# Kernel optimization log

Hardware: AMD Instinct MI355X
Metric: run time of the kernel (lower is better)

Reference implementation:

```python
import jax, jax.numpy as jnp
import numpy as np

DIM = 768
N_HEADS = 12
HEAD_DIM = DIM // N_HEADS
MLP_MULT = 4
EPS = 1e-5


def setup_inputs() -> dict:
    key = jax.random.key(0)
    ks = jax.random.split(key, 8)
    B, T = 2, 4096
    s = lambda fan_in: 1.0 / np.sqrt(fan_in)
    return {
        "x": jax.random.normal(ks[0], (B, T, DIM), dtype=jnp.float32),
        "ln1_w": jnp.ones((DIM,), jnp.float32),
        "ln1_b": jnp.zeros((DIM,), jnp.float32),
        # weights stored as (in, out): y = x @ W + b (equivalent to torch Linear)
        "w_qkv": jax.random.normal(ks[1], (DIM, 3 * DIM), jnp.float32) * s(DIM),
        "w_proj": jax.random.normal(ks[2], (DIM, DIM), jnp.float32) * s(DIM),
        "b_proj": jnp.zeros((DIM,), jnp.float32),
        "ln2_w": jnp.ones((DIM,), jnp.float32),
        "ln2_b": jnp.zeros((DIM,), jnp.float32),
        "w1": jax.random.normal(ks[3], (DIM, MLP_MULT * DIM), jnp.float32) * s(DIM),
        "b1": jnp.zeros((MLP_MULT * DIM,), jnp.float32),
        "w2": jax.random.normal(ks[4], (MLP_MULT * DIM, DIM), jnp.float32) * s(MLP_MULT * DIM),
        "b2": jnp.zeros((DIM,), jnp.float32),
    }


def _layernorm(x, w, b):
    mean = jnp.mean(x, axis=-1, keepdims=True)
    var = jnp.var(x, axis=-1, keepdims=True)
    return w * (x - mean) * jax.lax.rsqrt(var + EPS) + b


def reference(x, ln1_w, ln1_b, w_qkv, w_proj, b_proj, ln2_w, ln2_b, w1, b1, w2, b2):
    B, T, C = x.shape
    scale = HEAD_DIM ** -0.5

    # --- attention sub-block (pre-LN) ---
    h = _layernorm(x, ln1_w, ln1_b)
    qkv = h @ w_qkv                               # [B, T, 3C]
    q, k, v = jnp.split(qkv, 3, axis=-1)
    to_heads = lambda t: t.reshape(B, T, N_HEADS, HEAD_DIM).transpose(0, 2, 1, 3)
    q, k, v = to_heads(q), to_heads(k), to_heads(v)  # [B, H, T, D]

    att = jnp.einsum("bhqd,bhkd->bhqk", q, k) * scale  # full T x T scores
    causal = jnp.tril(jnp.ones((T, T), dtype=bool))
    att = jnp.where(causal, att, -jnp.inf)
    att = jax.nn.softmax(att, axis=-1)
    y = jnp.einsum("bhqk,bhkd->bhqd", att, v)          # [B, H, T, D]
    y = y.transpose(0, 2, 1, 3).reshape(B, T, C)
    y = y @ w_proj + b_proj
    x = x + y

    # --- MLP sub-block (pre-LN) ---
    h = _layernorm(x, ln2_w, ln2_b)
    h = jax.nn.gelu(h @ w1 + b1, approximate=False)
    h = h @ w2 + b2
    return x + h
```

## Files before the change

kernel.cpp:

```cpp
#include <hip/hip_runtime.h>

typedef unsigned short u16;
typedef __attribute__((ext_vector_type(4))) unsigned short u16x4;
typedef __attribute__((ext_vector_type(8))) short short8;
typedef __attribute__((ext_vector_type(4))) float f32x4;
typedef __attribute__((ext_vector_type(16))) float f32x16;

#define MFMA32(a, b, c) __builtin_amdgcn_mfma_f32_32x32x16_bf16(a, b, c, 0, 0, 0)

__device__ __forceinline__ u16 f2bf(float f) {
  union { float f; unsigned u; } x; x.f = f;
  unsigned r = x.u + 0x7fffu + ((x.u >> 16) & 1u);
  return (u16)(r >> 16);
}

__device__ __forceinline__ unsigned cvt_pk_bf16(float lo, float hi) {
  unsigned r;
  asm("v_cvt_pk_bf16_f32 %0, %1, %2" : "=v"(r) : "v"(lo), "v"(hi));
  return r;
}

__device__ __forceinline__ void load_lds16(const void* g, void* l) {
  __builtin_amdgcn_global_load_lds(
      (const __attribute__((address_space(1))) void*)g,
      (__attribute__((address_space(3))) void*)l,
      16, 0, 0);
}

__global__ __launch_bounds__(256) void transpose_k(const float* __restrict__ in,
                                                   u16* __restrict__ out,
                                                   int R, int C) {
  __shared__ float tile[32][33];
  const int tx = threadIdx.x & 31, ty = threadIdx.x >> 5;
  const int c0 = blockIdx.x * 32, r0 = blockIdx.y * 32;
#pragma unroll
  for (int i = 0; i < 4; ++i)
    tile[ty + i * 8][tx] = in[(size_t)(r0 + ty + i * 8) * C + c0 + tx];
  __syncthreads();
#pragma unroll
  for (int i = 0; i < 4; ++i)
    out[(size_t)(c0 + ty + i * 8) * R + r0 + tx] = f2bf(tile[tx][ty + i * 8]);
}

__global__ __launch_bounds__(256) void ln_k(const float* __restrict__ X,
                                            const float* __restrict__ w,
                                            const float* __restrict__ b,
                                            u16* __restrict__ O) {
  const int row = blockIdx.x;
  const float* xr = X + (size_t)row * 768;
  const int tid = threadIdx.x;
  float v0 = xr[tid], v1 = xr[tid + 256], v2 = xr[tid + 512];
  float s = v0 + v1 + v2;
  float s2 = v0 * v0 + v1 * v1 + v2 * v2;
#pragma unroll
  for (int m = 32; m; m >>= 1) { s += __shfl_xor(s, m); s2 += __shfl_xor(s2, m); }
  __shared__ float ps[4], ps2[4];
  if ((tid & 63) == 0) { ps[tid >> 6] = s; ps2[tid >> 6] = s2; }
  __syncthreads();
  s = ps[0] + ps[1] + ps[2] + ps[3];
  s2 = ps2[0] + ps2[1] + ps2[2] + ps2[3];
  const float mean = s * (1.f / 768.f);
  const float var = s2 * (1.f / 768.f) - mean * mean;
  const float rstd = rsqrtf(var + 1e-5f);
  u16* orow = O + (size_t)row * 768;
  orow[tid]       = f2bf((v0 - mean) * rstd * w[tid]       + b[tid]);
  orow[tid + 256] = f2bf((v1 - mean) * rstd * w[tid + 256] + b[tid + 256]);
  orow[tid + 512] = f2bf((v2 - mean) * rstd * w[tid + 512] + b[tid + 512]);
}

#define BM 128
#define BN 128
#define BKK 64

template <int EPI>
__global__ __launch_bounds__(256, 2) void gemm_k(
    const u16* __restrict__ A, const u16* __restrict__ Bt, int K, int N,
    const float* __restrict__ bias, const float* __restrict__ res,
    float* __restrict__ outF, u16* __restrict__ outB,
    u16* __restrict__ qout, u16* __restrict__ kout, u16* __restrict__ vout) {
  __shared__ __align__(16) u16 sA[BM * BKK];
  __shared__ __align__(16) u16 sB[BN * BKK];
  const int nTn = N / BN;
  const int nwg = gridDim.x;
  const int bid = ((int)blockIdx.x & 7) * (nwg >> 3) + ((int)blockIdx.x >> 3);
  const int tm = bid / nTn, tn = bid % nTn;
  const int m0 = tm * BM, n0 = tn * BN;
  const int tid = threadIdx.x, lane = tid & 63, wv = tid >> 6;
  const int wr = wv >> 1, wc = wv & 1;
  const int fr = lane & 15, fg = lane >> 4;

  const u16* aSrc[4];
  const u16* bSrc[4];
#pragma unroll
  for (int i = 0; i < 4; ++i) {
    int f = (i * 4 + wv) * 64 + lane;
    int r = f >> 3;
    int c = (f & 7) ^ (r & 7);
    aSrc[i] = A + (size_t)(m0 + r) * K + c * 8;
    bSrc[i] = Bt + (size_t)(n0 + r) * K + c * 8;
  }

  f32x4 acc[4][4];
#pragma unroll
  for (int m = 0; m < 4; ++m)
#pragma unroll
    for (int n = 0; n < 4; ++n) acc[m][n] = f32x4{0.f, 0.f, 0.f, 0.f};

  const int aswz = fr & 7;
  for (int kt = 0; kt < K; kt += BKK) {
#pragma unroll
    for (int i = 0; i < 4; ++i) {
      load_lds16(aSrc[i] + kt, (char*)sA + (i * 4 + wv) * 1024);
      load_lds16(bSrc[i] + kt, (char*)sB + (i * 4 + wv) * 1024);
    }
    __syncthreads();
#pragma unroll
    for (int ks = 0; ks < 2; ++ks) {
      const int c16 = (ks * 4 + fg) ^ aswz;
      short8 af[4], bf[4];
#pragma unroll
      for (int m = 0; m < 4; ++m)
        af[m] = *(const short8*)((const char*)sA +
                                 (((wr * 64 + m * 16 + fr) * 8 + c16) << 4));
#pragma unroll
      for (int n = 0; n < 4; ++n)
        bf[n] = *(const short8*)((const char*)sB +
                                 (((wc * 64 + n * 16 + fr) * 8 + c16) << 4));
#pragma unroll
      for (int m = 0; m < 4; ++m)
#pragma unroll
        for (int n = 0; n < 4; ++n)
          acc[m][n] =
              __builtin_amdgcn_mfma_f32_16x16x32_bf16(af[m], bf[n], acc[m][n], 0, 0, 0);
    }
    __syncthreads();
  }

#pragma unroll
  for (int m = 0; m < 4; ++m) {
    const int row = m0 + wr * 64 + m * 16 + fg * 4;
#pragma unroll
    for (int n = 0; n < 4; ++n) {
      const int col = n0 + wc * 64 + n * 16 + fr;
      f32x4 v = acc[m][n];
      if (EPI == 0) {
        const int part = (col >= 1536) ? 2 : (col >= 768 ? 1 : 0);
        const int cc = col - part * 768;
        const int hh = cc >> 6, dd = cc & 63;
        const int bb = row >> 12;
        const int t = row & 4095;
        const size_t bhh = (size_t)(bb * 12 + hh);
        if (part == 2) {
          u16x4 pk = {f2bf(v[0]), f2bf(v[1]), f2bf(v[2]), f2bf(v[3])};
          *(u16x4*)(vout + (bhh * 64 + dd) * 4096 + t) = pk;
        } else {
          const float qs = (part == 0) ? 0.18033688011112042f : 1.0f;
          u16* dst = (part == 0 ? qout : kout) + (bhh * 4096 + t) * 64 + dd;
#pragma unroll
          for (int r = 0; r < 4; ++r) dst[(size_t)r * 64] = f2bf(v[r] * qs);
        }
      } else if (EPI == 1) {
        const float bv = bias[col];
#pragma unroll
        for (int r = 0; r < 4; ++r)
          outF[(size_t)(row + r) * N + col] =
              v[r] + bv + res[(size_t)(row + r) * N + col];
      } else {
        const float bv = bias[col];
#pragma unroll
        for (int r = 0; r < 4; ++r) {
          float t = v[r] + bv;
          float g = 0.5f * t * (1.f + erff(t * 0.70710678118654752f));
          outB[(size_t)(row + r) * N + col] = f2bf(g);
        }
      }
    }
  }
}

__global__ __launch_bounds__(256) void attn_k(const u16* __restrict__ Q,
                                              const u16* __restrict__ Kb,
                                              const u16* __restrict__ Vt,
                                              u16* __restrict__ Y) {
  __shared__ __align__(16) u16 sK[2][64 * 64];
  __shared__ __align__(16) u16 sV[2][64 * 64];
  const int bid = blockIdx.x;
  const int qt = 31 - bid / 24;
  const int bh = bid % 24;
  const int bb = bh / 12, hh = bh - bb * 12;
  const int tid = threadIdx.x, lane = tid & 63, wv = tid >> 6;
  const int l31 = lane & 31, hi = lane >> 5;
  const int wq0 = qt * 128 + wv * 32;
  const int qG = wq0 + l31;
  const u16* Qh = Q + (size_t)bh * 4096 * 64;
  const u16* Kh = Kb + (size_t)bh * 4096 * 64;
  const u16* Vh = Vt + (size_t)bh * 64 * 4096;

  short8 qf[4];
#pragma unroll
  for (int ks = 0; ks < 4; ++ks)
    qf[ks] = *(const short8*)(Qh + (size_t)qG * 64 + ks * 16 + hi * 8);

  f32x16 yacc[2];
  yacc[0] = (f32x16)0.f;
  yacc[1] = (f32x16)0.f;
  float lrun = 0.f;

  const u16* kSrc[2];
  const u16* vSrc[2];
  int dstOff[2];
#pragma unroll
  for (int i = 0; i < 2; ++i) {
    const int f = i * 256 + tid;
    const int su = f >> 5, l = f & 31;
    const int ks_ = su >> 2, c2 = (su >> 1) & 1, h_ = su & 1;
    kSrc[i] = Kh + (size_t)(c2 * 32 + l) * 64 + ks_ * 16 + h_ * 8;
    vSrc[i] = Vh + (size_t)(c2 * 32 + l) * 4096 + ks_ * 16 + h_ * 8;
    dstOff[i] = f * 16;
  }

#define STAGE(buf, cc)                                                         \
  do {                                                                         \
    _Pragma("unroll") for (int i_ = 0; i_ < 2; ++i_) {                         \
      load_lds16(kSrc[i_] + (size_t)(cc)*4096, (char*)sK[buf] + dstOff[i_]);   \
      load_lds16(vSrc[i_] + (size_t)(cc)*64, (char*)sV[buf] + dstOff[i_]);     \
    }                                                                          \
  } while (0)

  const int nch = 2 * qt + 2;
  STAGE(0, 0);
  __syncthreads();

  const int rdBase = hi * 512 + l31 * 16;

  for (int c = 0; c < nch; ++c) {
    const int kb = c * 64;
    const int cur = c & 1;
    if (c + 1 < nch) STAGE(cur ^ 1, c + 1);

    if (kb <= wq0 + 31) {
      f32x16 s[2];
      s[0] = (f32x16)0.f;
      s[1] = (f32x16)0.f;
#pragma unroll
      for (int ks = 0; ks < 4; ++ks) {
#pragma unroll
        for (int kc = 0; kc < 2; ++kc) {
          short8 kf = *(const short8*)((const char*)sK[cur] +
                                       (ks * 2048 + kc * 1024 + rdBase));
          s[kc] = MFMA32(kf, qf[ks], s[kc]);
        }
      }

      if (kb + 63 > wq0) {
#pragma unroll
        for (int kc = 0; kc < 2; ++kc)
#pragma unroll
          for (int r = 0; r < 16; ++r) {
            const int key = kb + kc * 32 + (r & 3) + 8 * (r >> 2) + 4 * hi;
            if (key > qG) s[kc][r] = -3e38f;
          }
      }

#pragma unroll
      for (int kc = 0; kc < 2; ++kc)
#pragma unroll
        for (int r = 0; r < 16; ++r)
          s[kc][r] = __builtin_amdgcn_exp2f(s[kc][r] - 8.f);

      float u[8];
#pragma unroll
      for (int i = 0; i < 8; ++i)
        u[i] = (s[0][i] + s[0][i + 8]) + (s[1][i] + s[1][i + 8]);
#pragma unroll
      for (int st = 4; st; st >>= 1)
#pragma unroll
        for (int i = 0; i < st; ++i) u[i] += u[i + st];
      lrun += u[0] + __shfl_xor(u[0], 32);

#pragma unroll
      for (int ks2 = 0; ks2 < 4; ++ks2) {
        const int kc = ks2 >> 1, rb = (ks2 & 1) * 8;
        unsigned W0 = cvt_pk_bf16(s[kc][rb + 0], s[kc][rb + 1]);
        unsigned W1 = cvt_pk_bf16(s[kc][rb + 2], s[kc][rb + 3]);
        unsigned W2 = cvt_pk_bf16(s[kc][rb + 4], s[kc][rb + 5]);
        unsigned W3 = cvt_pk_bf16(s[kc][rb + 6], s[kc][rb + 7]);
        asm("v_permlane32_swap_b32 %0, %1" : "+v"(W0), "+v"(W2));
        asm("v_permlane32_swap_b32 %0, %1" : "+v"(W1), "+v"(W3));
        union { unsigned w[4]; short8 v; } pb;
        pb.w[0] = W0; pb.w[1] = W1; pb.w[2] = W2; pb.w[3] = W3;
#pragma unroll
        for (int dt = 0; dt < 2; ++dt) {
          short8 vf = *(const short8*)((const char*)sV[cur] +
                                       (ks2 * 2048 + dt * 1024 + rdBase));
          yacc[dt] = MFMA32(vf, pb.v, yacc[dt]);
        }
      }
    }
    __syncthreads();
  }

  const float inv = 1.f / lrun;
  u16* Yr = Y + (size_t)(bb * 4096 + qt * 128 + wv * 32 + l31) * 768 + hh * 64;
#pragma unroll
  for (int dt = 0; dt < 2; ++dt)
#pragma unroll
    for (int g = 0; g < 4; ++g) {
      u16x4 pk = {f2bf(yacc[dt][g * 4 + 0] * inv), f2bf(yacc[dt][g * 4 + 1] * inv),
                  f2bf(yacc[dt][g * 4 + 2] * inv), f2bf(yacc[dt][g * 4 + 3] * inv)};
      *(u16x4*)(Yr + dt * 32 + g * 8 + hi * 4) = pk;
    }
}

extern "C" void kernel_launch(void* const* d_in, const int* in_sizes, int n_in,
                              void* d_out, int out_size, void* d_ws, size_t ws_size,
                              hipStream_t stream) {
  const float* x = (const float*)d_in[0];
  const float* ln1w = (const float*)d_in[1];
  const float* ln1b = (const float*)d_in[2];
  const float* wqkv = (const float*)d_in[3];
  const float* wproj = (const float*)d_in[4];
  const float* bproj = (const float*)d_in[5];
  const float* ln2w = (const float*)d_in[6];
  const float* ln2b = (const float*)d_in[7];
  const float* w1 = (const float*)d_in[8];
  const float* b1 = (const float*)d_in[9];
  const float* w2 = (const float*)d_in[10];
  const float* b2 = (const float*)d_in[11];
  float* out = (float*)d_out;
  char* ws = (char*)d_ws;

  const size_t SZ_ACT = (size_t)8192 * 768 * 2;
  u16* hbuf = (u16*)(ws);
  u16* qb = (u16*)(ws + SZ_ACT);
  u16* kb = (u16*)(ws + 2 * SZ_ACT);
  u16* vT = (u16*)(ws + 3 * SZ_ACT);
  u16* ybuf = (u16*)(ws + 4 * SZ_ACT);
  float* out1 = (float*)(ws + 5 * SZ_ACT);
  char* wsw = ws + 5 * SZ_ACT + (size_t)8192 * 768 * 4;
  u16* wqkvT = (u16*)(wsw);
  u16* wprojT = (u16*)(wsw + 3538944);
  u16* w1T = (u16*)(wsw + 3538944 + 1179648);
  u16* w2T = (u16*)(wsw + 3538944 + 1179648 + 4718592);
  u16* h3 = hbuf;
  u16* h2 = ybuf;

  transpose_k<<<dim3(2304 / 32, 768 / 32), 256, 0, stream>>>(wqkv, wqkvT, 768, 2304);
  transpose_k<<<dim3(768 / 32, 768 / 32), 256, 0, stream>>>(wproj, wprojT, 768, 768);
  transpose_k<<<dim3(3072 / 32, 768 / 32), 256, 0, stream>>>(w1, w1T, 768, 3072);
  transpose_k<<<dim3(768 / 32, 3072 / 32), 256, 0, stream>>>(w2, w2T, 3072, 768);

  ln_k<<<8192, 256, 0, stream>>>(x, ln1w, ln1b, hbuf);

  gemm_k<0><<<64 * (2304 / 128), 256, 0, stream>>>(hbuf, wqkvT, 768, 2304,
      nullptr, nullptr, nullptr, nullptr, qb, kb, vT);

  attn_k<<<768, 256, 0, stream>>>(qb, kb, vT, ybuf);

  gemm_k<1><<<64 * (768 / 128), 256, 0, stream>>>(ybuf, wprojT, 768, 768,
      bproj, x, out1, nullptr, nullptr, nullptr, nullptr);

  ln_k<<<8192, 256, 0, stream>>>(out1, ln2w, ln2b, h2);

  gemm_k<2><<<64 * (3072 / 128), 256, 0, stream>>>(h2, w1T, 768, 3072,
      b1, nullptr, nullptr, h3, nullptr, nullptr, nullptr);

  gemm_k<1><<<64 * (768 / 128), 256, 0, stream>>>(h3, w2T, 3072, 768,
      b2, out1, out, nullptr, nullptr, nullptr, nullptr);

  (void)in_sizes; (void)n_in; (void)out_size; (void)ws_size;
}
```

Before: 303.1 us.

## Pre-tile K/V in LDS-ready layout, widen attention chunks to 128 keys

```diff
diff --git a/kernel.cpp b/kernel.cpp
--- a/kernel.cpp
+++ b/kernel.cpp
@@ -151,11 +151,24 @@
         const int t = row & 4095;
         const size_t bhh = (size_t)(bb * 12 + hh);
         if (part == 2) {
+          const int ks_ = (t & 63) >> 4, h_ = (t >> 3) & 1, e0 = t & 7;
           u16x4 pk = {f2bf(v[0]), f2bf(v[1]), f2bf(v[2]), f2bf(v[3])};
-          *(u16x4*)(vout + (bhh * 64 + dd) * 4096 + t) = pk;
+          *(u16x4*)(vout + bhh * 262144 + (size_t)(t >> 6) * 4096 +
+                    (size_t)(((ks_ << 2) + ((dd >> 5) << 1) + h_) * 256 +
+                             (dd & 31) * 8 + e0)) = pk;
+        } else if (part == 1) {
+          const int ks_ = dd >> 4, h_ = (dd >> 3) & 1, e = dd & 7;
+          u16* base = kout + bhh * 262144;
+#pragma unroll
+          for (int r = 0; r < 4; ++r) {
+            const int t2 = t + r;
+            base[(size_t)(t2 >> 6) * 4096 +
+                 (size_t)((((ks_ << 2) + (((t2 & 63) >> 5) << 1) + h_) * 256) +
+                          (t2 & 31) * 8 + e)] = f2bf(v[r]);
+          }
         } else {
-          const float qs = (part == 0) ? 0.18033688011112042f : 1.0f;
-          u16* dst = (part == 0 ? qout : kout) + (bhh * 4096 + t) * 64 + dd;
+          const float qs = 0.18033688011112042f;
+          u16* dst = qout + (bhh * 4096 + t) * 64 + dd;
 #pragma unroll
           for (int r = 0; r < 4; ++r) dst[(size_t)r * 64] = f2bf(v[r] * qs);
         }
@@ -182,8 +195,8 @@
                                               const u16* __restrict__ Kb,
                                               const u16* __restrict__ Vt,
                                               u16* __restrict__ Y) {
-  __shared__ __align__(16) u16 sK[2][64 * 64];
-  __shared__ __align__(16) u16 sV[2][64 * 64];
+  __shared__ __align__(16) u16 sK[2][8192];
+  __shared__ __align__(16) u16 sV[2][8192];
   const int bid = blockIdx.x;
   const int qt = 31 - bid / 24;
   const int bh = bid % 24;
@@ -193,8 +206,8 @@
   const int wq0 = qt * 128 + wv * 32;
   const int qG = wq0 + l31;
   const u16* Qh = Q + (size_t)bh * 4096 * 64;
-  const u16* Kh = Kb + (size_t)bh * 4096 * 64;
-  const u16* Vh = Vt + (size_t)bh * 64 * 4096;
+  const u16* Kh = Kb + (size_t)bh * 262144;
+  const u16* Vh = Vt + (size_t)bh * 262144;
 
   short8 qf[4];
 #pragma unroll
@@ -206,94 +219,92 @@
   yacc[1] = (f32x16)0.f;
   float lrun = 0.f;
 
-  const u16* kSrc[2];
-  const u16* vSrc[2];
-  int dstOff[2];
-#pragma unroll
-  for (int i = 0; i < 2; ++i) {
-    const int f = i * 256 + tid;
-    const int su = f >> 5, l = f & 31;
-    const int ks_ = su >> 2, c2 = (su >> 1) & 1, h_ = su & 1;
-    kSrc[i] = Kh + (size_t)(c2 * 32 + l) * 64 + ks_ * 16 + h_ * 8;
-    vSrc[i] = Vh + (size_t)(c2 * 32 + l) * 4096 + ks_ * 16 + h_ * 8;
-    dstOff[i] = f * 16;
-  }
-
 #define STAGE(buf, cc)                                                         \
   do {                                                                         \
-    _Pragma("unroll") for (int i_ = 0; i_ < 2; ++i_) {                         \
-      load_lds16(kSrc[i_] + (size_t)(cc)*4096, (char*)sK[buf] + dstOff[i_]);   \
-      load_lds16(vSrc[i_] + (size_t)(cc)*64, (char*)sV[buf] + dstOff[i_]);     \
+    const u16* gk_ = Kh + (size_t)(cc)*8192;                                   \
+    const u16* gv_ = Vh + (size_t)(cc)*8192;                                   \
+    _Pragma("unroll") for (int i_ = 0; i_ < 4; ++i_) {                         \
+      const int f_ = i_ * 256 + tid;                                           \
+      load_lds16(gk_ + f_ * 8, (char*)sK[buf] + f_ * 16);                      \
+      load_lds16(gv_ + f_ * 8, (char*)sV[buf] + f_ * 16);                      \
     }                                                                          \
   } while (0)
 
-  const int nch = 2 * qt + 2;
+  const int nch = qt + 1;
   STAGE(0, 0);
   __syncthreads();
 
   const int rdBase = hi * 512 + l31 * 16;
 
   for (int c = 0; c < nch; ++c) {
-    const int kb = c * 64;
     const int cur = c & 1;
     if (c + 1 < nch) STAGE(cur ^ 1, c + 1);
 
-    if (kb <= wq0 + 31) {
-      f32x16 s[2];
-      s[0] = (f32x16)0.f;
-      s[1] = (f32x16)0.f;
-#pragma unroll
-      for (int ks = 0; ks < 4; ++ks) {
-#pragma unroll
-        for (int kc = 0; kc < 2; ++kc) {
-          short8 kf = *(const short8*)((const char*)sK[cur] +
-                                       (ks * 2048 + kc * 1024 + rdBase));
-          s[kc] = MFMA32(kf, qf[ks], s[kc]);
-        }
-      }
-
-      if (kb + 63 > wq0) {
+#pragma unroll
+    for (int hf = 0; hf < 2; ++hf) {
+      const int kb = c * 128 + hf * 64;
+      if (kb <= wq0 + 31) {
+        const char* sKb = (const char*)sK[cur] + hf * 8192;
+        const char* sVb = (const char*)sV[cur] + hf * 8192;
+
+        f32x16 s[2];
+        s[0] = (f32x16)0.f;
+        s[1] = (f32x16)0.f;
+        __builtin_amdgcn_s_setprio(1);
+#pragma unroll
+        for (int ks = 0; ks < 4; ++ks) {
+#pragma unroll
+          for (int kc = 0; kc < 2; ++kc) {
+            short8 kf = *(const short8*)(sKb + ks * 2048 + kc * 1024 + rdBase);
+            s[kc] = MFMA32(kf, qf[ks], s[kc]);
+          }
+        }
+        __builtin_amdgcn_s_setprio(0);
+
+        if (kb + 63 > wq0) {
+#pragma unroll
+          for (int kc = 0; kc < 2; ++kc)
+#pragma unroll
+            for (int r = 0; r < 16; ++r) {
+              const int key = kb + kc * 32 + (r & 3) + 8 * (r >> 2) + 4 * hi;
+              if (key > qG) s[kc][r] = -3e38f;
+            }
+        }
+
 #pragma unroll
         for (int kc = 0; kc < 2; ++kc)
 #pragma unroll
-          for (int r = 0; r < 16; ++r) {
-            const int key = kb + kc * 32 + (r & 3) + 8 * (r >> 2) + 4 * hi;
-            if (key > qG) s[kc][r] = -3e38f;
+          for (int r = 0; r < 16; ++r)
+            s[kc][r] = __builtin_amdgcn_exp2f(s[kc][r] - 8.f);
+
+        float u[8];
+#pragma unroll
+        for (int i = 0; i < 8; ++i)
+          u[i] = (s[0][i] + s[0][i + 8]) + (s[1][i] + s[1][i + 8]);
+#pragma unroll
+        for (int st = 4; st; st >>= 1)
+#pragma unroll
+          for (int i = 0; i < st; ++i) u[i] += u[i + st];
+        lrun += u[0] + __shfl_xor(u[0], 32);
+
+#pragma unroll
+        for (int ks2 = 0; ks2 < 4; ++ks2) {
+          const int kc = ks2 >> 1, rb = (ks2 & 1) * 8;
+          unsigned W0 = cvt_pk_bf16(s[kc][rb + 0], s[kc][rb + 1]);
+          unsigned W1 = cvt_pk_bf16(s[kc][rb + 2], s[kc][rb + 3]);
+          unsigned W2 = cvt_pk_bf16(s[kc][rb + 4], s[kc][rb + 5]);
+          unsigned W3 = cvt_pk_bf16(s[kc][rb + 6], s[kc][rb + 7]);
+          asm("v_permlane32_swap_b32 %0, %1" : "+v"(W0), "+v"(W2));
+          asm("v_permlane32_swap_b32 %0, %1" : "+v"(W1), "+v"(W3));
+          union { unsigned w[4]; short8 v; } pb;
+          pb.w[0] = W0; pb.w[1] = W1; pb.w[2] = W2; pb.w[3] = W3;
+          __builtin_amdgcn_s_setprio(1);
+#pragma unroll
+          for (int dt = 0; dt < 2; ++dt) {
+            short8 vf = *(const short8*)(sVb + ks2 * 2048 + dt * 1024 + rdBase);
+            yacc[dt] = MFMA32(vf, pb.v, yacc[dt]);
           }
-      }
-
-#pragma unroll
-      for (int kc = 0; kc < 2; ++kc)
-#pragma unroll
-        for (int r = 0; r < 16; ++r)
-          s[kc][r] = __builtin_amdgcn_exp2f(s[kc][r] - 8.f);
-
-      float u[8];
-#pragma unroll
-      for (int i = 0; i < 8; ++i)
-        u[i] = (s[0][i] + s[0][i + 8]) + (s[1][i] + s[1][i + 8]);
-#pragma unroll
-      for (int st = 4; st; st >>= 1)
-#pragma unroll
-        for (int i = 0; i < st; ++i) u[i] += u[i + st];
-      lrun += u[0] + __shfl_xor(u[0], 32);
-
-#pragma unroll
-      for (int ks2 = 0; ks2 < 4; ++ks2) {
-        const int kc = ks2 >> 1, rb = (ks2 & 1) * 8;
-        unsigned W0 = cvt_pk_bf16(s[kc][rb + 0], s[kc][rb + 1]);
-        unsigned W1 = cvt_pk_bf16(s[kc][rb + 2], s[kc][rb + 3]);
-        unsigned W2 = cvt_pk_bf16(s[kc][rb + 4], s[kc][rb + 5]);
-        unsigned W3 = cvt_pk_bf16(s[kc][rb + 6], s[kc][rb + 7]);
-        asm("v_permlane32_swap_b32 %0, %1" : "+v"(W0), "+v"(W2));
-        asm("v_permlane32_swap_b32 %0, %1" : "+v"(W1), "+v"(W3));
-        union { unsigned w[4]; short8 v; } pb;
-        pb.w[0] = W0; pb.w[1] = W1; pb.w[2] = W2; pb.w[3] = W3;
-#pragma unroll
-        for (int dt = 0; dt < 2; ++dt) {
-          short8 vf = *(const short8*)((const char*)sV[cur] +
-                                       (ks2 * 2048 + dt * 1024 + rdBase));
-          yacc[dt] = MFMA32(vf, pb.v, yacc[dt]);
+          __builtin_amdgcn_s_setprio(0);
         }
       }
     }
```

Result: faster. 279.8 us (-7.7%).
